# Optimization experiments

Measured on AMD Instinct MI355X. Metric: run time of the kernel, lower is better.

Reference implementation:

```python
import jax, jax.numpy as jnp
import numpy as np

B, L, D = 8, 8192, 512
TARGET_RATIO = 1.0 / 6.0


def _normalize(v):
    # matches torch F.normalize(dim=-1, eps=1e-12)
    n = jnp.maximum(jnp.linalg.norm(v, axis=-1, keepdims=True), 1e-12)
    return v / n


def _downsample(x, b_hard):
    # vectorized stream compaction, padded to L (static upper bound of L_max)
    Bb, Ll, Dd = x.shape
    cnt = jnp.cumsum(b_hard.astype(jnp.int32), axis=1)
    pos = jnp.where(b_hard > 0.5, cnt - 1, Ll)          # non-selected -> dump slot L
    bidx = jnp.arange(Bb)[:, None]
    out = jnp.zeros((Bb, Ll + 1, Dd), x.dtype).at[bidx, pos].set(x)[:, :Ll]
    counts = cnt[:, -1]
    mask = jnp.arange(Ll)[None, :] < counts[:, None]
    return out, mask


def setup_inputs() -> dict:
    key = jax.random.key(0)
    k1, k2, k3 = jax.random.split(key, 3)
    x = jax.random.normal(k1, (B, L, D), jnp.float32)
    W_q = jax.random.normal(k2, (D, D), jnp.float32) / np.sqrt(D)
    W_k = jax.random.normal(k3, (D, D), jnp.float32) / np.sqrt(D)
    return {"x": x, "W_q": W_q, "W_k": W_k}


def reference(x, W_q, W_k):
    q = _normalize(jnp.einsum('bld,ed->ble', x, W_q))   # nn.Linear: x @ W.T
    k = _normalize(jnp.einsum('bld,ed->ble', x, W_k))
    k_prev = jnp.pad(k[:, :-1, :], ((0, 0), (1, 0), (0, 0)))
    cos_sim = jnp.sum(q * k_prev, axis=-1)               # (B, L)
    p = jnp.clip(0.5 * (1.0 - cos_sim), 0.0, 1.0)
    p = p.at[:, 0].set(1.0)                              # first position always boundary
    b_hard = (p >= 0.5).astype(x.dtype)
    N = 1.0 / TARGET_RATIO
    F_actual = jnp.mean(b_hard)
    G_actual = jnp.mean(p)
    ratio_loss = N / (N - 1.0) * ((N - 1.0) * F_actual * G_actual + (1.0 - F_actual) * (1.0 - G_actual))
    compressed, comp_mask = _downsample(x, b_hard)
    p_compressed, _ = _downsample(p[..., None], b_hard)
    p_compressed = p_compressed[..., 0]
    return (compressed, comp_mask, b_hard, p, p_compressed, ratio_loss)
```

## Files before the change

### kernel.cpp

```cpp
#include <hip/hip_runtime.h>
#include <hip/hip_bf16.h>
#include <math.h>

#define BB 8
#define LL 8192
#define DD 512
#define NROWS (BB * LL)

#define OUT_COMP   0
#define OUT_MASK   33554432
#define OUT_BHARD  33619968
#define OUT_P      33685504
#define OUT_PCOMP  33751040
#define OUT_LOSS   33816576

#define WS_FIXLIST 0
#define WS_FIXCNT  262144
#define WS_COUNTS  262148
#define WS_SUMP    262180
#define WS_SEL     262212
#define WS_SSK     524416
#define WS_SSQ     786560
#define WS_DOT     1048704
#define WS_WQH     1310848
#define WS_WQL     1835136
#define WS_WKH     2359424
#define WS_WKL     2883712

#define FIX_CAP 65536
#define FIX_TAU 2e-4f

typedef __attribute__((ext_vector_type(8))) short short8;
typedef __attribute__((ext_vector_type(4))) float f32x4;

static __device__ __forceinline__ short bf16_hi(float x) {
  __hip_bfloat16 h = __float2bfloat16(x);
  return __builtin_bit_cast(short, h);
}
static __device__ __forceinline__ float bf16_back(short s) {
  __hip_bfloat16 h = __builtin_bit_cast(__hip_bfloat16, s);
  return __bfloat162float(h);
}

static __device__ __forceinline__ void ld_g2l16(const void* g, void* l) {
  __builtin_amdgcn_global_load_lds(
      (const __attribute__((address_space(1))) void*)g,
      (__attribute__((address_space(3))) void*)l, 16, 0, 0);
}

__global__ __launch_bounds__(256) void wsplit(
    const float* __restrict__ Wq, const float* __restrict__ Wk,
    short* __restrict__ wqh, short* __restrict__ wql,
    short* __restrict__ wkh, short* __restrict__ wkl,
    float* __restrict__ ssk, float* __restrict__ ssq,
    float* __restrict__ dotb, int* __restrict__ fixcnt) {
  const int t = blockIdx.x * 256 + threadIdx.x;
  if (t == 0) *fixcnt = 0;
  ssk[t] = 0.0f;
  ssq[t] = 0.0f;
  dotb[t] = 0.0f;

  const int m = t >> 15;
  const int c = t & 32767;
  const int kt = c >> 11;
  const int ct = (c >> 6) & 31;
  const int l = c & 63;
  const int n = l & 15;
  const int kblk = l >> 4;
  const int e = ct * 16 + n;
  const int d0 = kt * 32 + kblk * 8;
  const float* src = (m ? Wk : Wq) + (long)e * 512 + d0;
  short* dh = (m ? wkh : wqh) + (long)c * 8;
  short* dl = (m ? wkl : wql) + (long)c * 8;
  float4 v0 = *(const float4*)src;
  float4 v1 = *(const float4*)(src + 4);
  float av[8] = {v0.x, v0.y, v0.z, v0.w, v1.x, v1.y, v1.z, v1.w};
  short8 hi, lo;
#pragma unroll
  for (int j = 0; j < 8; ++j) {
    short hh = bf16_hi(av[j]);
    hi[j] = hh;
    lo[j] = bf16_hi(av[j] - bf16_back(hh));
  }
  *(short8*)dh = hi;
  *(short8*)dl = lo;
}

template <int PASS>
__global__ __launch_bounds__(256, 2) void gemm_tile(
    const float* __restrict__ x, const short* __restrict__ wh,
    const short* __restrict__ wl, float* __restrict__ kbuf,
    float* __restrict__ ssOut, float* __restrict__ dotOut) {
  __shared__ uint4 smem4[2048];
  short* AH = (short*)smem4;
  short* AL = AH + 4096;
  short* BH = AL + 4096;
  short* BL = BH + 4096;

  const int tid = threadIdx.x;
  const int lane = tid & 63;
  const int w = tid >> 6;
  const int wrow = w & 1, wcol = w >> 1;
  const int g = lane >> 4, n = lane & 15;
  const int bx = blockIdx.x;
  const int rb = bx >> 2, cb = bx & 3;
  const long r0 = (long)rb * 128;

  const int m128 = tid >> 1, h = tid & 1;
  const int mbs = m128 >> 4, ms = m128 & 15;
  const float* xrow = x + (r0 + m128) * 512 + h * 16;
  short* paH = AH + ((mbs * 4 + 2 * h) * 16 + ms) * 8;
  short* paL = AL + ((mbs * 4 + 2 * h) * 16 + ms) * 8;

  f32x4 acc[4][4];
#pragma unroll
  for (int mb = 0; mb < 4; ++mb)
#pragma unroll
    for (int nb = 0; nb < 4; ++nb) acc[mb][nb] = (f32x4){0.f, 0.f, 0.f, 0.f};

  float4 f0 = *(const float4*)(xrow + 0);
  float4 f1 = *(const float4*)(xrow + 4);
  float4 f2 = *(const float4*)(xrow + 8);
  float4 f3 = *(const float4*)(xrow + 12);

  for (int kt = 0; kt < 16; ++kt) {
    const long bbase = ((long)(kt * 32 + cb * 8) << 9) + w * 1024 + lane * 8;
    ld_g2l16(wh + bbase, BH + w * 1024);
    ld_g2l16(wh + bbase + 512, BH + w * 1024 + 512);
    ld_g2l16(wl + bbase, BL + w * 1024);
    ld_g2l16(wl + bbase + 512, BL + w * 1024 + 512);
    {
      float av[16] = {f0.x, f0.y, f0.z, f0.w, f1.x, f1.y, f1.z, f1.w,
                      f2.x, f2.y, f2.z, f2.w, f3.x, f3.y, f3.z, f3.w};
      short8 h0, h1, l0, l1;
#pragma unroll
      for (int j = 0; j < 8; ++j) {
        short a = bf16_hi(av[j]);
        h0[j] = a;
        l0[j] = bf16_hi(av[j] - bf16_back(a));
        short b = bf16_hi(av[8 + j]);
        h1[j] = b;
        l1[j] = bf16_hi(av[8 + j] - bf16_back(b));
      }
      *(short8*)paH = h0;
      *(short8*)(paH + 128) = h1;
      *(short8*)paL = l0;
      *(short8*)(paL + 128) = l1;
    }
    __syncthreads();
    if (kt < 15) {
      const float* xp = xrow + (kt + 1) * 32;
      f0 = *(const float4*)(xp + 0);
      f1 = *(const float4*)(xp + 4);
      f2 = *(const float4*)(xp + 8);
      f3 = *(const float4*)(xp + 12);
    }
    short8 ah[4], al[4], bh[4], bl[4];
#pragma unroll
    for (int mb = 0; mb < 4; ++mb) {
      const int ar = (((wrow * 4 + mb) & 3) * 64 + lane) * 8;
      ah[mb] = *(const short8*)(AH + ((wrow * 4 + mb) * 64 % 4096) + 0 * 0 + ar * 0);
      (void)ar;
    }
#pragma unroll
    for (int mb = 0; mb < 4; ++mb) {
      const int cm = wrow * 4 + mb;
      ah[mb] = *(const short8*)(AH + (cm * 64 + lane) * 8 % 4096);
      al[mb] = *(const short8*)(AL + (cm * 64 + lane) * 8 % 4096);
    }
#pragma unroll
    for (int nb = 0; nb < 4; ++nb) {
      bh[nb] = *(const short8*)(BH + ((wcol * 4 + nb) * 64 + lane) * 8);
      bl[nb] = *(const short8*)(BL + ((wcol * 4 + nb) * 64 + lane) * 8);
    }
#pragma unroll
    for (int nb = 0; nb < 4; ++nb)
#pragma unroll
      for (int mb = 0; mb < 4; ++mb) {
        acc[mb][nb] = __builtin_amdgcn_mfma_f32_16x16x32_bf16(ah[mb], bh[nb], acc[mb][nb], 0, 0, 0);
        acc[mb][nb] = __builtin_amdgcn_mfma_f32_16x16x32_bf16(al[mb], bh[nb], acc[mb][nb], 0, 0, 0);
        acc[mb][nb] = __builtin_amdgcn_mfma_f32_16x16x32_bf16(ah[mb], bl[nb], acc[mb][nb], 0, 0, 0);
      }
    __syncthreads();
  }

  const int colbase = cb * 128 + wcol * 64 + n;
#pragma unroll
  for (int mb = 0; mb < 4; ++mb) {
#pragma unroll
    for (int reg = 0; reg < 4; ++reg) {
      const long row = r0 + wrow * 64 + mb * 16 + g * 4 + reg;
      float ss = 0.f, dt = 0.f;
      const long rp = (row > 0) ? row - 1 : 0;
#pragma unroll
      for (int nb = 0; nb < 4; ++nb) {
        float v = acc[mb][nb][reg];
        ss = fmaf(v, v, ss);
        if (PASS == 1) {
          kbuf[row * 512 + colbase + nb * 16] = v;
        } else {
          float kp = kbuf[rp * 512 + colbase + nb * 16];
          dt = fmaf(v, kp, dt);
        }
      }
#pragma unroll
      for (int m = 1; m < 16; m <<= 1) {
        ss += __shfl_xor(ss, m, 64);
        if (PASS == 2) dt += __shfl_xor(dt, m, 64);
      }
      if (n == 0) {
        atomicAdd(&ssOut[row], ss);
        if (PASS == 2) atomicAdd(&dotOut[row], dt);
      }
    }
  }
}

__global__ __launch_bounds__(256) void combine(
    const float* __restrict__ ssq, const float* __restrict__ ssk,
    const float* __restrict__ dotb, float* __restrict__ dout,
    int* __restrict__ fixlist, int* __restrict__ fixcnt) {
  const int r = blockIdx.x * 256 + threadIdx.x;
  const int l = r & (LL - 1);
  float p;
  float cosv = 0.0f;
  if (l != 0) {
    float nq = fmaxf(sqrtf(ssq[r]), 1e-12f);
    float nk = fmaxf(sqrtf(ssk[r - 1]), 1e-12f);
    cosv = dotb[r] / (nq * nk);
    p = fminf(fmaxf(0.5f * (1.0f - cosv), 0.0f), 1.0f);
  } else {
    p = 1.0f;
  }
  dout[OUT_P + r] = p;
  dout[OUT_BHARD + r] = (p >= 0.5f) ? 1.0f : 0.0f;
  if (l != 0 && fabsf(cosv) < FIX_TAU) {
    int idx = atomicAdd(fixcnt, 1);
    if (idx < FIX_CAP) fixlist[idx] = r;
  }
}

__global__ __launch_bounds__(256) void fixup(
    const float* __restrict__ x, const float* __restrict__ Wq,
    const float* __restrict__ Wk, float* __restrict__ dout,
    const int* __restrict__ fixlist, const int* __restrict__ fixcnt) {
  __shared__ float xr[512], xp[512];
  __shared__ double red[3][256];
  const int t = threadIdx.x;
  int nfix = *fixcnt;
  if (nfix > FIX_CAP) nfix = FIX_CAP;

  for (int idx = blockIdx.x; idx < nfix; idx += gridDim.x) {
    const int r = fixlist[idx];
    for (int d = t; d < 512; d += 256) {
      xr[d] = x[(long)r * 512 + d];
      xp[d] = x[(long)(r - 1) * 512 + d];
    }
    __syncthreads();
    double ssq = 0.0, ssk = 0.0, dot = 0.0;
    for (int e = t; e < 512; e += 256) {
      const float* wq = Wq + (long)e * 512;
      const float* wk = Wk + (long)e * 512;
      double q = 0.0, k = 0.0;
      for (int d = 0; d < 512; ++d) {
        q = fma((double)xr[d], (double)wq[d], q);
        k = fma((double)xp[d], (double)wk[d], k);
      }
      ssq += q * q;
      ssk += k * k;
      dot += q * k;
    }
    red[0][t] = ssq;
    red[1][t] = ssk;
    red[2][t] = dot;
    __syncthreads();
    for (int s = 128; s > 0; s >>= 1) {
      if (t < s) {
        red[0][t] += red[0][t + s];
        red[1][t] += red[1][t + s];
        red[2][t] += red[2][t + s];
      }
      __syncthreads();
    }
    if (t == 0) {
      double nq = sqrt(red[0][0]);
      double nk = sqrt(red[1][0]);
      if (nq < 1e-12) nq = 1e-12;
      if (nk < 1e-12) nk = 1e-12;
      float c = (float)(red[2][0] / (nq * nk));
      float p = fminf(fmaxf(0.5f * (1.0f - c), 0.0f), 1.0f);
      dout[OUT_P + r] = p;
      dout[OUT_BHARD + r] = (p >= 0.5f) ? 1.0f : 0.0f;
    }
    __syncthreads();
  }
}

__global__ __launch_bounds__(256) void scanb(
    float* __restrict__ dout, int* __restrict__ sel,
    int* __restrict__ counts, float* __restrict__ sump) {
  __shared__ int wtot[4];
  __shared__ float wps[4];
  const int b = blockIdx.x;
  const int t = threadIdx.x;
  const int lane = t & 63, wv = t >> 6;
  const long base = (long)b * LL;

  int cnt = 0;
  float psum = 0.0f;
#pragma unroll 4
  for (int j = 0; j < 32; ++j) {
    int l = t * 32 + j;
    float bh = dout[OUT_BHARD + base + l];
    float pv = dout[OUT_P + base + l];
    cnt += (bh > 0.5f) ? 1 : 0;
    psum += pv;
  }
  int inc = cnt;
#pragma unroll
  for (int off = 1; off < 64; off <<= 1) {
    int u = __shfl_up(inc, off, 64);
    if (lane >= off) inc += u;
  }
  float ps = psum;
#pragma unroll
  for (int off = 1; off < 64; off <<= 1) ps += __shfl_xor(ps, off, 64);
  if (lane == 63) wtot[wv] = inc;
  if (lane == 0) wps[wv] = ps;
  __syncthreads();
  int wbase = 0, total = 0;
#pragma unroll
  for (int i = 0; i < 4; ++i) {
    int c = wtot[i];
    if (i < wv) wbase += c;
    total += c;
  }
  if (t == 0) {
    counts[b] = total;
    sump[b] = wps[0] + wps[1] + wps[2] + wps[3];
  }
  for (int j = 0; j < 32; ++j) {
    int l = t * 32 + j;
    dout[OUT_MASK + base + l] = (l < total) ? 1.0f : 0.0f;
    dout[OUT_PCOMP + base + l] = 0.0f;
  }
  __syncthreads();
  int pos = wbase + inc - cnt;
  for (int j = 0; j < 32; ++j) {
    int l = t * 32 + j;
    float bh = dout[OUT_BHARD + base + l];
    if (bh > 0.5f) {
      dout[OUT_PCOMP + base + pos] = dout[OUT_P + base + l];
      sel[base + pos] = l;
      ++pos;
    }
  }
}

__global__ void lossk(float* __restrict__ dout, const int* __restrict__ counts,
                      const float* __restrict__ sump) {
  if (threadIdx.x == 0 && blockIdx.x == 0) {
    float fc = 0.0f, gs = 0.0f;
    for (int b = 0; b < BB; ++b) {
      fc += (float)counts[b];
      gs += sump[b];
    }
    float F = fc / (float)NROWS;
    float G = gs / (float)NROWS;
    dout[OUT_LOSS] = 1.2f * (5.0f * F * G + (1.0f - F) * (1.0f - G));
  }
}

__global__ __launch_bounds__(128) void emit(
    const float* __restrict__ x, float* __restrict__ dout,
    const int* __restrict__ sel, const int* __restrict__ counts) {
  const long bid = blockIdx.x;
  const int b = (int)(bid >> 13);
  const int j = (int)(bid & (LL - 1));
  const int cnt = counts[b];
  float4 v = make_float4(0.0f, 0.0f, 0.0f, 0.0f);
  if (j < cnt) {
    const int l = sel[((long)b << 13) + j];
    v = *(const float4*)(x + (((long)b << 13) + l) * 512 + threadIdx.x * 4);
  }
  *(float4*)(dout + OUT_COMP + (((long)b << 13) + j) * 512 + threadIdx.x * 4) = v;
}

extern "C" void kernel_launch(void* const* d_in, const int* in_sizes, int n_in,
                              void* d_out, int out_size, void* d_ws,
                              size_t ws_size, hipStream_t stream) {
  const float* x = (const float*)d_in[0];
  const float* Wq = (const float*)d_in[1];
  const float* Wk = (const float*)d_in[2];
  float* out = (float*)d_out;
  char* ws = (char*)d_ws;

  int* fixlist = (int*)(ws + WS_FIXLIST);
  int* fixcnt = (int*)(ws + WS_FIXCNT);
  int* counts = (int*)(ws + WS_COUNTS);
  float* sump = (float*)(ws + WS_SUMP);
  int* sel = (int*)(ws + WS_SEL);
  float* ssk = (float*)(ws + WS_SSK);
  float* ssq = (float*)(ws + WS_SSQ);
  float* dotb = (float*)(ws + WS_DOT);
  short* wqh = (short*)(ws + WS_WQH);
  short* wql = (short*)(ws + WS_WQL);
  short* wkh = (short*)(ws + WS_WKH);
  short* wkl = (short*)(ws + WS_WKL);

  float* kbuf = out + OUT_COMP;

  wsplit<<<256, 256, 0, stream>>>(Wq, Wk, wqh, wql, wkh, wkl, ssk, ssq, dotb, fixcnt);
  gemm_tile<1><<<2048, 256, 0, stream>>>(x, wkh, wkl, kbuf, ssk, nullptr);
  gemm_tile<2><<<2048, 256, 0, stream>>>(x, wqh, wql, kbuf, ssq, dotb);
  combine<<<NROWS / 256, 256, 0, stream>>>(ssq, ssk, dotb, out, fixlist, fixcnt);
  fixup<<<512, 256, 0, stream>>>(x, Wq, Wk, out, fixlist, fixcnt);
  scanb<<<BB, 256, 0, stream>>>(out, sel, counts, sump);
  lossk<<<1, 64, 0, stream>>>(out, counts, sump);
  emit<<<NROWS, 128, 0, stream>>>(x, out, sel, counts);
}
```

Before: 550.3 us.

## Switch split-precision GEMM from bf16 to fp16 and store k intermediate as fp16

Replaces the bf16 hi/lo split with an fp16 hi/lo split for both weights and activations, using fp16 MFMA instructions. Because fp16 keeps more mantissa bits, the fixup threshold drops so fewer rows are sent to the exact recompute path. The k intermediate buffer is stored as fp16, halving its write and read traffic between the two GEMM passes. The A-tile LDS store layout is also simplified to contiguous per-thread writes. The risk is fp16 range limits on the x values and the residual, plus reduced precision in the stored k.

```diff
diff --git a/kernel.cpp b/kernel.cpp
--- a/kernel.cpp
+++ b/kernel.cpp
@@ -28,19 +28,10 @@
 #define WS_WKL     2883712
 
 #define FIX_CAP 65536
-#define FIX_TAU 2e-4f
-
-typedef __attribute__((ext_vector_type(8))) short short8;
+#define FIX_TAU 1e-4f
+
+typedef __attribute__((ext_vector_type(8))) _Float16 half8;
 typedef __attribute__((ext_vector_type(4))) float f32x4;
-
-static __device__ __forceinline__ short bf16_hi(float x) {
-  __hip_bfloat16 h = __float2bfloat16(x);
-  return __builtin_bit_cast(short, h);
-}
-static __device__ __forceinline__ float bf16_back(short s) {
-  __hip_bfloat16 h = __builtin_bit_cast(__hip_bfloat16, s);
-  return __bfloat162float(h);
-}
 
 static __device__ __forceinline__ void ld_g2l16(const void* g, void* l) {
   __builtin_amdgcn_global_load_lds(
@@ -50,8 +41,8 @@
 
 __global__ __launch_bounds__(256) void wsplit(
     const float* __restrict__ Wq, const float* __restrict__ Wk,
-    short* __restrict__ wqh, short* __restrict__ wql,
-    short* __restrict__ wkh, short* __restrict__ wkl,
+    _Float16* __restrict__ wqh, _Float16* __restrict__ wql,
+    _Float16* __restrict__ wkh, _Float16* __restrict__ wkl,
     float* __restrict__ ssk, float* __restrict__ ssq,
     float* __restrict__ dotb, int* __restrict__ fixcnt) {
   const int t = blockIdx.x * 256 + threadIdx.x;
@@ -70,32 +61,32 @@
   const int e = ct * 16 + n;
   const int d0 = kt * 32 + kblk * 8;
   const float* src = (m ? Wk : Wq) + (long)e * 512 + d0;
-  short* dh = (m ? wkh : wqh) + (long)c * 8;
-  short* dl = (m ? wkl : wql) + (long)c * 8;
+  _Float16* dh = (m ? wkh : wqh) + (long)c * 8;
+  _Float16* dl = (m ? wkl : wql) + (long)c * 8;
   float4 v0 = *(const float4*)src;
   float4 v1 = *(const float4*)(src + 4);
   float av[8] = {v0.x, v0.y, v0.z, v0.w, v1.x, v1.y, v1.z, v1.w};
-  short8 hi, lo;
+  half8 hi, lo;
 #pragma unroll
   for (int j = 0; j < 8; ++j) {
-    short hh = bf16_hi(av[j]);
+    _Float16 hh = (_Float16)av[j];
     hi[j] = hh;
-    lo[j] = bf16_hi(av[j] - bf16_back(hh));
-  }
-  *(short8*)dh = hi;
-  *(short8*)dl = lo;
+    lo[j] = (_Float16)(av[j] - (float)hh);
+  }
+  *(half8*)dh = hi;
+  *(half8*)dl = lo;
 }
 
 template <int PASS>
 __global__ __launch_bounds__(256, 2) void gemm_tile(
-    const float* __restrict__ x, const short* __restrict__ wh,
-    const short* __restrict__ wl, float* __restrict__ kbuf,
+    const float* __restrict__ x, const _Float16* __restrict__ wh,
+    const _Float16* __restrict__ wl, _Float16* __restrict__ kbuf,
     float* __restrict__ ssOut, float* __restrict__ dotOut) {
-  __shared__ uint4 smem4[2048];
-  short* AH = (short*)smem4;
-  short* AL = AH + 4096;
-  short* BH = AL + 4096;
-  short* BL = BH + 4096;
+  __shared__ _Float16 smem[16384];
+  _Float16* AH = smem;
+  _Float16* AL = AH + 4096;
+  _Float16* BH = AL + 4096;
+  _Float16* BL = BH + 4096;
 
   const int tid = threadIdx.x;
   const int lane = tid & 63;
@@ -106,11 +97,9 @@
   const int rb = bx >> 2, cb = bx & 3;
   const long r0 = (long)rb * 128;
 
-  const int m128 = tid >> 1, h = tid & 1;
-  const int mbs = m128 >> 4, ms = m128 & 15;
-  const float* xrow = x + (r0 + m128) * 512 + h * 16;
-  short* paH = AH + ((mbs * 4 + 2 * h) * 16 + ms) * 8;
-  short* paL = AL + ((mbs * 4 + 2 * h) * 16 + ms) * 8;
+  const int arow = ((tid >> 6) << 4) | (tid & 15);
+  const int akb = (tid >> 4) & 3;
+  const float* ap = x + (r0 + arow) * 512 + akb * 8;
 
   f32x4 acc[4][4];
 #pragma unroll
@@ -118,10 +107,10 @@
 #pragma unroll
     for (int nb = 0; nb < 4; ++nb) acc[mb][nb] = (f32x4){0.f, 0.f, 0.f, 0.f};
 
-  float4 f0 = *(const float4*)(xrow + 0);
-  float4 f1 = *(const float4*)(xrow + 4);
-  float4 f2 = *(const float4*)(xrow + 8);
-  float4 f3 = *(const float4*)(xrow + 12);
+  float4 f0 = *(const float4*)(ap);
+  float4 f1 = *(const float4*)(ap + 4);
+  float4 f2 = *(const float4*)(ap + 64 * 512);
+  float4 f3 = *(const float4*)(ap + 64 * 512 + 4);
 
   for (int kt = 0; kt < 16; ++kt) {
     const long bbase = ((long)(kt * 32 + cb * 8) << 9) + w * 1024 + lane * 8;
@@ -130,56 +119,50 @@
     ld_g2l16(wl + bbase, BL + w * 1024);
     ld_g2l16(wl + bbase + 512, BL + w * 1024 + 512);
     {
-      float av[16] = {f0.x, f0.y, f0.z, f0.w, f1.x, f1.y, f1.z, f1.w,
-                      f2.x, f2.y, f2.z, f2.w, f3.x, f3.y, f3.z, f3.w};
-      short8 h0, h1, l0, l1;
+      float av0[8] = {f0.x, f0.y, f0.z, f0.w, f1.x, f1.y, f1.z, f1.w};
+      float av1[8] = {f2.x, f2.y, f2.z, f2.w, f3.x, f3.y, f3.z, f3.w};
+      half8 h0, h1, l0, l1;
 #pragma unroll
       for (int j = 0; j < 8; ++j) {
-        short a = bf16_hi(av[j]);
+        _Float16 a = (_Float16)av0[j];
         h0[j] = a;
-        l0[j] = bf16_hi(av[j] - bf16_back(a));
-        short b = bf16_hi(av[8 + j]);
+        l0[j] = (_Float16)(av0[j] - (float)a);
+        _Float16 b = (_Float16)av1[j];
         h1[j] = b;
-        l1[j] = bf16_hi(av[8 + j] - bf16_back(b));
-      }
-      *(short8*)paH = h0;
-      *(short8*)(paH + 128) = h1;
-      *(short8*)paL = l0;
-      *(short8*)(paL + 128) = l1;
+        l1[j] = (_Float16)(av1[j] - (float)b);
+      }
+      *(half8*)(AH + tid * 8) = h0;
+      *(half8*)(AH + (tid + 256) * 8) = h1;
+      *(half8*)(AL + tid * 8) = l0;
+      *(half8*)(AL + (tid + 256) * 8) = l1;
     }
     __syncthreads();
     if (kt < 15) {
-      const float* xp = xrow + (kt + 1) * 32;
-      f0 = *(const float4*)(xp + 0);
+      const float* xp = ap + (kt + 1) * 32;
+      f0 = *(const float4*)(xp);
       f1 = *(const float4*)(xp + 4);
-      f2 = *(const float4*)(xp + 8);
-      f3 = *(const float4*)(xp + 12);
-    }
-    short8 ah[4], al[4], bh[4], bl[4];
-#pragma unroll
-    for (int mb = 0; mb < 4; ++mb) {
-      const int ar = (((wrow * 4 + mb) & 3) * 64 + lane) * 8;
-      ah[mb] = *(const short8*)(AH + ((wrow * 4 + mb) * 64 % 4096) + 0 * 0 + ar * 0);
-      (void)ar;
-    }
+      f2 = *(const float4*)(xp + 64 * 512);
+      f3 = *(const float4*)(xp + 64 * 512 + 4);
+    }
+    half8 ah[4], al[4], bh[4], bl[4];
 #pragma unroll
     for (int mb = 0; mb < 4; ++mb) {
       const int cm = wrow * 4 + mb;
-      ah[mb] = *(const short8*)(AH + (cm * 64 + lane) * 8 % 4096);
-      al[mb] = *(const short8*)(AL + (cm * 64 + lane) * 8 % 4096);
+      ah[mb] = *(const half8*)(AH + (cm * 64 + lane) * 8);
+      al[mb] = *(const half8*)(AL + (cm * 64 + lane) * 8);
     }
 #pragma unroll
     for (int nb = 0; nb < 4; ++nb) {
-      bh[nb] = *(const short8*)(BH + ((wcol * 4 + nb) * 64 + lane) * 8);
-      bl[nb] = *(const short8*)(BL + ((wcol * 4 + nb) * 64 + lane) * 8);
+      bh[nb] = *(const half8*)(BH + ((wcol * 4 + nb) * 64 + lane) * 8);
+      bl[nb] = *(const half8*)(BL + ((wcol * 4 + nb) * 64 + lane) * 8);
     }
 #pragma unroll
     for (int nb = 0; nb < 4; ++nb)
 #pragma unroll
       for (int mb = 0; mb < 4; ++mb) {
-        acc[mb][nb] = __builtin_amdgcn_mfma_f32_16x16x32_bf16(ah[mb], bh[nb], acc[mb][nb], 0, 0, 0);
-        acc[mb][nb] = __builtin_amdgcn_mfma_f32_16x16x32_bf16(al[mb], bh[nb], acc[mb][nb], 0, 0, 0);
-        acc[mb][nb] = __builtin_amdgcn_mfma_f32_16x16x32_bf16(ah[mb], bl[nb], acc[mb][nb], 0, 0, 0);
+        acc[mb][nb] = __builtin_amdgcn_mfma_f32_16x16x32_f16(ah[mb], bh[nb], acc[mb][nb], 0, 0, 0);
+        acc[mb][nb] = __builtin_amdgcn_mfma_f32_16x16x32_f16(al[mb], bh[nb], acc[mb][nb], 0, 0, 0);
+        acc[mb][nb] = __builtin_amdgcn_mfma_f32_16x16x32_f16(ah[mb], bl[nb], acc[mb][nb], 0, 0, 0);
       }
     __syncthreads();
   }
@@ -197,9 +180,9 @@
         float v = acc[mb][nb][reg];
         ss = fmaf(v, v, ss);
         if (PASS == 1) {
-          kbuf[row * 512 + colbase + nb * 16] = v;
+          kbuf[row * 512 + colbase + nb * 16] = (_Float16)v;
         } else {
-          float kp = kbuf[rp * 512 + colbase + nb * 16];
+          float kp = (float)kbuf[rp * 512 + colbase + nb * 16];
           dt = fmaf(v, kp, dt);
         }
       }
@@ -403,12 +386,12 @@
   float* ssk = (float*)(ws + WS_SSK);
   float* ssq = (float*)(ws + WS_SSQ);
   float* dotb = (float*)(ws + WS_DOT);
-  short* wqh = (short*)(ws + WS_WQH);
-  short* wql = (short*)(ws + WS_WQL);
-  short* wkh = (short*)(ws + WS_WKH);
-  short* wkl = (short*)(ws + WS_WKL);
-
-  float* kbuf = out + OUT_COMP;
+  _Float16* wqh = (_Float16*)(ws + WS_WQH);
+  _Float16* wql = (_Float16*)(ws + WS_WQL);
+  _Float16* wkh = (_Float16*)(ws + WS_WKH);
+  _Float16* wkl = (_Float16*)(ws + WS_WKL);
+
+  _Float16* kbuf = (_Float16*)(out + OUT_COMP);
 
   wsplit<<<256, 256, 0, stream>>>(Wq, Wk, wqh, wql, wkh, wkl, ssk, ssq, dotb, fixcnt);
   gemm_tile<1><<<2048, 256, 0, stream>>>(x, wkh, wkl, kbuf, ssk, nullptr);
```

New measurement: 545.0 us. About the same (-1.0%).
